# Kernel optimization log

Hardware: AMD Instinct MI355X
Metric: run time of the kernel (lower is better)

Reference implementation:

```python
import jax, jax.numpy as jnp
import numpy as np

FACTOR = 5


def setup_inputs() -> dict:
    key = jax.random.key(0)
    k1, k2, k3, k4 = jax.random.split(key, 4)
    B, L, H, D = 2, 4096, 8, 64
    sample_k = min(FACTOR * int(np.ceil(np.log(L))), L)  # 45
    return {
        "queries": jax.random.normal(k1, (B, L, H, D), dtype=jnp.float32),
        "keys": jax.random.normal(k2, (B, L, H, D), dtype=jnp.float32),
        "values": jax.random.normal(k3, (B, L, H, D), dtype=jnp.float32),
        "attn_mask": jnp.zeros((1,), dtype=bool),  # unused; ProbMask is built internally
        "index_sample": jax.random.randint(k4, (L, sample_k), 0, L, dtype=jnp.int32),
    }


def reference(queries, keys, values, attn_mask, index_sample):
    # queries/keys/values: [B, L, H, D] -> [B, H, L, D]
    Q = jnp.swapaxes(queries, 1, 2)
    K = jnp.swapaxes(keys, 1, 2)
    V = jnp.swapaxes(values, 1, 2)
    B, H, L_Q, D = Q.shape
    L_K = K.shape[2]
    n_top = min(FACTOR * int(np.ceil(np.log(L_Q))), L_Q)
    scale = 1.0 / jnp.sqrt(jnp.float32(D))

    # --- sparse measurement: sampled QK scores ---
    # K_sample[b,h,q,s,d] = K[b,h,index_sample[q,s],d]
    K_sample = K[:, :, index_sample, :]                       # [B,H,L_Q,S,D]
    QK_sample = jnp.einsum("bhqd,bhqsd->bhqs", Q, K_sample)   # [B,H,L_Q,S]
    M = QK_sample.max(axis=-1) - QK_sample.sum(axis=-1) / L_K  # sparsity measure

    # --- top-u query selection ---
    _, M_top = jax.lax.top_k(M, n_top)                         # [B,H,u]
    Q_reduce = jnp.take_along_axis(Q, M_top[..., None], axis=2)  # [B,H,u,D]

    # --- full scores for selected queries ---
    scores = jnp.einsum("bhud,bhkd->bhuk", Q_reduce, K) * scale  # [B,H,u,L_K]

    # mask_flag=True: causal ProbMask (key pos > selected query pos)
    key_pos = jnp.arange(L_K)
    causal = key_pos[None, None, None, :] > M_top[..., None]
    scores = jnp.where(causal, -jnp.inf, scores)
    attn = jax.nn.softmax(scores, axis=-1)

    # --- initial context (cumsum, masked case) + scatter update ---
    context = jnp.cumsum(V, axis=2)                            # [B,H,L_Q,D]
    ctx_sel = jnp.einsum("bhuk,bhkd->bhud", attn, V)
    b_idx = jnp.arange(B)[:, None, None]
    h_idx = jnp.arange(H)[None, :, None]
    context = context.at[b_idx, h_idx, M_top].set(ctx_sel)
    return jnp.swapaxes(context, 1, 2)  # [B, L_Q, H, D]
```

## Files before the change

kernel.cpp:

```cpp
#include <hip/hip_runtime.h>
#include <math.h>

#define B_    2
#define L_    4096
#define H_    8
#define D_    64
#define S_    45
#define NT_   45
#define BH_   16
#define CHV   64
#define NCHV  64
#define KC    128
#define NKC   32
#define SCALE 0.125f
#define NEG_BIG (-1e30f)

#define OFF_M     0
#define OFF_MTOP  65536
#define OFF_MPART 66304
#define OFF_SPART 89344
#define OFF_CTXP  112384
#define OFF_VSUM  1586944

template <int CTRL>
__device__ __forceinline__ float dpp_ror_f(float x) {
    int y = __builtin_amdgcn_update_dpp(0, __float_as_int(x), CTRL, 0xF, 0xF, false);
    return __int_as_float(y);
}

__device__ __forceinline__ unsigned short f2bf(float x) {
    return (unsigned short)(__float_as_uint(x) >> 16);
}
__device__ __forceinline__ float bflo(unsigned u) { return __uint_as_float(u << 16); }
__device__ __forceinline__ float bfhi(unsigned u) { return __uint_as_float(u & 0xffff0000u); }

__global__ __launch_bounds__(256) void k1(const float* __restrict__ Q,
                                          const float* __restrict__ Kt,
                                          const float* __restrict__ V,
                                          const int* __restrict__ samp,
                                          float* __restrict__ ws)
{
    int tid  = threadIdx.x;
    int w    = tid >> 6;
    int lane = tid & 63;

    if (blockIdx.x < 4096) {
        int i   = blockIdx.x;
        int xcd = i & 7;
        int b   = xcd >> 2;
        int hh  = (xcd >> 1) & 1;
        int qq  = ((i >> 3) << 1) | (xcd & 1);

        __shared__ int soff[4][S_];
        if (tid < 4 * S_) {
            int qs = tid / S_, ss = tid - qs * S_;
            soff[qs][ss] = (samp[(qq * 4 + qs) * S_ + ss] << 11) | (hh << 10);
        }
        __syncthreads();

        int q  = qq * 4 + w;
        int h4 = lane >> 4;

        const float4 q4 = *(const float4*)(Q +
            ((((long)b * L_ + q) * H_ + hh * 4) << 6) + lane * 4);

        const char* kslab = (const char*)Kt + (long)b * (L_ * 2048);
        unsigned lb = (unsigned)(lane * 16);

        float mx = NEG_BIG, sm = 0.f;
#pragma unroll
        for (int jb = 0; jb < 45; jb += 15) {
            float4 kb[15];
#pragma unroll
            for (int j = 0; j < 15; ++j)
                kb[j] = *(const float4*)(kslab +
                        ((unsigned)soff[w][jb + j] + lb));
#pragma unroll
            for (int j = 0; j < 15; ++j) {
                float p = q4.x * kb[j].x + q4.y * kb[j].y +
                          q4.z * kb[j].z + q4.w * kb[j].w;
                p += dpp_ror_f<0x121>(p);
                p += dpp_ror_f<0x122>(p);
                p += dpp_ror_f<0x124>(p);
                p += dpp_ror_f<0x128>(p);
                mx = fmaxf(mx, p);
                sm += p;
            }
        }
        if ((lane & 15) == 0)
            ws[OFF_M + ((long)(b * 8 + hh * 4 + h4)) * L_ + q] =
                mx - sm * (1.0f / (float)L_);
    } else {
        int unit = (blockIdx.x - 4096) * 4 + w;
        int bh = unit >> 6, ch = unit & 63;
        int b = bh >> 3, h = bh & 7;
        const float* vp = V + ((((long)b * L_ + (long)ch * CHV) * H_ + h) << 6) + lane;
        float ssum = 0.f;
#pragma unroll
        for (int ib = 0; ib < CHV; ib += 16) {
            float vb[16];
#pragma unroll
            for (int j = 0; j < 16; ++j) vb[j] = vp[(long)(ib + j) * (H_ * D_)];
#pragma unroll
            for (int j = 0; j < 16; ++j) ssum += vb[j];
        }
        ws[OFF_VSUM + unit * 64 + lane] = ssum;
    }
}

__global__ __launch_bounds__(256) void k2(float* __restrict__ ws)
{
    int tid  = threadIdx.x;
    int w    = tid >> 6;
    int lane = tid & 63;

    int bh = blockIdx.x;
    int* Mtop = (int*)ws + OFF_MTOP + bh * NT_;

    __shared__ float lv_[4][NT_];
    __shared__ int   li_[4][NT_];

    const float4* m4 = (const float4*)(ws + OFF_M + (long)bh * L_ +
                                       w * 1024 + lane * 16);
    float vals[16];
    {
        float4 a = m4[0], bq = m4[1], c = m4[2], d = m4[3];
        vals[0]=a.x; vals[1]=a.y; vals[2]=a.z; vals[3]=a.w;
        vals[4]=bq.x; vals[5]=bq.y; vals[6]=bq.z; vals[7]=bq.w;
        vals[8]=c.x; vals[9]=c.y; vals[10]=c.z; vals[11]=c.w;
        vals[12]=d.x; vals[13]=d.y; vals[14]=d.z; vals[15]=d.w;
    }
    float lv = NEG_BIG; int li = lane * 16;
#pragma unroll
    for (int j = 0; j < 16; ++j)
        if (vals[j] > lv) { lv = vals[j]; li = lane * 16 + j; }

    for (int r = 0; r < NT_; ++r) {
        float rm = lv;
        rm = fmaxf(rm, dpp_ror_f<0x121>(rm));
        rm = fmaxf(rm, dpp_ror_f<0x122>(rm));
        rm = fmaxf(rm, dpp_ror_f<0x124>(rm));
        rm = fmaxf(rm, dpp_ror_f<0x128>(rm));
        rm = fmaxf(rm, __shfl_xor(rm, 16));
        rm = fmaxf(rm, __shfl_xor(rm, 32));
        unsigned long long bm = __ballot(lv == rm);
        int winner = __ffsll(bm) - 1;
        int wi = __shfl(li, winner);
        if (lane == 0) { lv_[w][r] = rm; li_[w][r] = w * 1024 + wi; }
        if (lane == winner) {
#pragma unroll
            for (int j = 0; j < 16; ++j)
                if (j == (wi & 15)) vals[j] = NEG_BIG;
            lv = NEG_BIG; li = lane * 16;
#pragma unroll
            for (int j = 0; j < 16; ++j)
                if (vals[j] > lv) { lv = vals[j]; li = lane * 16 + j; }
        }
    }
    __syncthreads();

    if (w == 0) {
        int g = lane & 3;
        int p = 0;
        float hv = lv_[g][0]; int hi = li_[g][0];
        for (int r = 0; r < NT_; ++r) {
            float v0 = __shfl(hv, 0), v1 = __shfl(hv, 1),
                  v2 = __shfl(hv, 2), v3 = __shfl(hv, 3);
            int   i0 = __shfl(hi, 0), i1 = __shfl(hi, 1),
                  i2 = __shfl(hi, 2), i3 = __shfl(hi, 3);
            float bv = v0; int bi = i0, bg = 0;
            if (v1 > bv) { bv = v1; bi = i1; bg = 1; }
            if (v2 > bv) { bv = v2; bi = i2; bg = 2; }
            if (v3 > bv) { bv = v3; bi = i3; bg = 3; }
            if (lane == 0) Mtop[r] = bi;
            if (g == bg) {
                ++p;
                hv = (p < NT_) ? lv_[g][p] : NEG_BIG;
                hi = (p < NT_) ? li_[g][p] : 0;
            }
        }
    }
}

#define KPAD16 72
#define NUH    23
__global__ __launch_bounds__(256) void k3(const float* __restrict__ Q,
                                          const float* __restrict__ Kt,
                                          const float* __restrict__ V,
                                          float* __restrict__ out,
                                          float* __restrict__ ws)
{
    __shared__ unsigned short Klds16[KC * KPAD16];
    __shared__ unsigned short P16[NUH * KC];
    __shared__ int qpos[NUH];

    int tid = threadIdx.x;

    if (blockIdx.x < 1024) {
        int bh = blockIdx.x >> 6;
        int kc = (blockIdx.x >> 1) & 31;
        int ug = blockIdx.x & 1;
        int b = bh >> 3, h = bh & 7;
        int kbase = kc * KC;
        int u0 = ug * 23;
        int NU = ug ? 22 : 23;

        if (tid < NU) qpos[tid] = ((const int*)ws)[OFF_MTOP + bh * NT_ + tid + u0];

        {
            const float4* ksrc4 = (const float4*)(Kt + ((((long)b * L_ + kbase) * H_ + h) << 6));
#pragma unroll
            for (int i = 0; i < 8; ++i) {
                int e = i * 256 + tid;
                int r = e >> 4, c4 = e & 15;
                float4 kv = ksrc4[(long)r * (H_ * D_ / 4) + c4];
                uint2 pk;
                pk.x = (__float_as_uint(kv.x) >> 16) | (__float_as_uint(kv.y) & 0xffff0000u);
                pk.y = (__float_as_uint(kv.z) >> 16) | (__float_as_uint(kv.w) & 0xffff0000u);
                *(uint2*)&Klds16[r * KPAD16 + c4 * 4] = pk;
            }
        }
        __syncthreads();

        int k = tid & 127, uh = tid >> 7;
        int kpos = kbase + k;
        {
            float kf[64];
#pragma unroll
            for (int j = 0; j < 8; ++j) {
                uint4 U = *(const uint4*)&Klds16[k * KPAD16 + j * 8];
                kf[j*8+0] = bflo(U.x); kf[j*8+1] = bfhi(U.x);
                kf[j*8+2] = bflo(U.y); kf[j*8+3] = bfhi(U.y);
                kf[j*8+4] = bflo(U.z); kf[j*8+5] = bfhi(U.z);
                kf[j*8+6] = bflo(U.w); kf[j*8+7] = bfhi(U.w);
            }

#pragma unroll 3
            for (int j = 0; j < 12; ++j) {
                int ul = uh * 12 + j;
                if (ul > NU - 1) ul = NU - 1;
                int qp_ = __builtin_amdgcn_readfirstlane(qpos[ul]);
                const float4* qrow = (const float4*)(Q + ((((long)b * L_ + qp_) * H_ + h) << 6));
                float a0 = 0.f, a1 = 0.f, a2 = 0.f, a3 = 0.f;
#pragma unroll
                for (int jj = 0; jj < 16; jj += 4) {
                    float4 q0 = qrow[jj + 0], q1 = qrow[jj + 1];
                    float4 q2 = qrow[jj + 2], q3 = qrow[jj + 3];
                    a0 += q0.x * kf[jj*4+ 0] + q0.y * kf[jj*4+ 1] +
                          q0.z * kf[jj*4+ 2] + q0.w * kf[jj*4+ 3];
                    a1 += q1.x * kf[jj*4+ 4] + q1.y * kf[jj*4+ 5] +
                          q1.z * kf[jj*4+ 6] + q1.w * kf[jj*4+ 7];
                    a2 += q2.x * kf[jj*4+ 8] + q2.y * kf[jj*4+ 9] +
                          q2.z * kf[jj*4+10] + q2.w * kf[jj*4+11];
                    a3 += q3.x * kf[jj*4+12] + q3.y * kf[jj*4+13] +
                          q3.z * kf[jj*4+14] + q3.w * kf[jj*4+15];
                }
                float sc = ((a0 + a1) + (a2 + a3)) * SCALE;
                if (kpos > qp_) sc = NEG_BIG;
                P16[ul * KC + k] = f2bf(sc);
            }
        }
        __syncthreads();

        int lane = tid & 63, w = tid >> 6;
        for (int ul = w; ul < NU; ul += 4) {
            float s0 = bflo(P16[ul * KC + lane]);
            float s1 = bflo(P16[ul * KC + 64 + lane]);
            float m = fmaxf(s0, s1);
#pragma unroll
            for (int off = 32; off; off >>= 1) m = fmaxf(m, __shfl_xor(m, off));
            float e0 = __expf(s0 - m), e1 = __expf(s1 - m);
            unsigned short b0 = f2bf(e0), b1 = f2bf(e1);
            P16[ul * KC + lane]      = b0;
            P16[ul * KC + 64 + lane] = b1;
            float sm = bflo(b0) + bflo(b1);
#pragma unroll
            for (int off = 32; off; off >>= 1) sm += __shfl_xor(sm, off);
            if (lane == 0) {
                ws[OFF_MPART + ((long)bh * NT_ + u0 + ul) * NKC + kc] = m;
                ws[OFF_SPART + ((long)bh * NT_ + u0 + ul) * NKC + kc] = sm;
            }
        }
        __syncthreads();

        {
            const float* vsrc = V + ((((long)b * L_ + kbase) * H_ + h) << 6);
            float ctx[6];
#pragma unroll
            for (int j = 0; j < 6; ++j) ctx[j] = 0.f;
            for (int kk8 = 0; kk8 < 16; ++kk8) {
                float v[8];
#pragma unroll
                for (int t = 0; t < 8; ++t)
                    v[t] = vsrc[(long)(kk8 * 8 + t) * (H_ * D_) + lane];
#pragma unroll
                for (int j = 0; j < 6; ++j) {
                    int ul = w + j * 4;
                    if (ul < NU) {
                        uint4 U = *(const uint4*)&P16[ul * KC + kk8 * 8];
                        ctx[j] += bflo(U.x) * v[0] + bfhi(U.x) * v[1]
                                + bflo(U.y) * v[2] + bfhi(U.y) * v[3]
                                + bflo(U.z) * v[4] + bfhi(U.z) * v[5]
                                + bflo(U.w) * v[6] + bfhi(U.w) * v[7];
                    }
                }
            }
#pragma unroll
            for (int j = 0; j < 6; ++j) {
                int ul = w + j * 4;
                if (ul < NU)
                    ws[OFF_CTXP + ((long)(bh * NKC + kc) * NT_ + u0 + ul) * 64 + lane] = ctx[j];
            }
        }
    } else {
        int w    = tid >> 6;
        int lane = tid & 63;
        int unit = (blockIdx.x - 1024) * 4 + w;
        int bh = unit >> 6, ch = unit & 63;
        int b = bh >> 3, h = bh & 7;
        int d = lane;

        float acc = 0.f;
        {
            const float* vs = ws + OFF_VSUM + (long)bh * NCHV * 64 + d;
            int c = 0;
            for (; c + 8 <= ch; c += 8) {
                float vb[8];
#pragma unroll
                for (int j = 0; j < 8; ++j) vb[j] = vs[(c + j) * 64];
#pragma unroll
                for (int j = 0; j < 8; ++j) acc += vb[j];
            }
            for (; c < ch; ++c) acc += vs[c * 64];
        }

        const float* vp = V   + ((((long)b * L_ + (long)ch * CHV) * H_ + h) << 6) + d;
        float*       op = out + ((((long)b * L_ + (long)ch * CHV) * H_ + h) << 6) + d;
#pragma unroll
        for (int ib = 0; ib < CHV; ib += 16) {
            float vb[16];
#pragma unroll
            for (int j = 0; j < 16; ++j) vb[j] = vp[(long)(ib + j) * (H_ * D_)];
#pragma unroll
            for (int j = 0; j < 16; ++j) {
                acc += vb[j];
                op[(long)(ib + j) * (H_ * D_)] = acc;
            }
        }
    }
}

__global__ __launch_bounds__(64) void kD(float* __restrict__ out,
                                         const float* __restrict__ ws)
{
    int lane = threadIdx.x;
    int unit = blockIdx.x;
    int bh = unit / NT_, u = unit - bh * NT_;
    int b = bh >> 3, h = bh & 7;

    const float4* mp4 = (const float4*)(ws + OFF_MPART + ((long)bh * NT_ + u) * NKC);
    const float4* sp4 = (const float4*)(ws + OFF_SPART + ((long)bh * NT_ + u) * NKC);

    float mc[NKC], sc[NKC];
    float m = NEG_BIG;
#pragma unroll
    for (int c4 = 0; c4 < NKC / 4; ++c4) {
        float4 mv = mp4[c4];
        float4 sv = sp4[c4];
        mc[c4 * 4 + 0] = mv.x; mc[c4 * 4 + 1] = mv.y;
        mc[c4 * 4 + 2] = mv.z; mc[c4 * 4 + 3] = mv.w;
        sc[c4 * 4 + 0] = sv.x; sc[c4 * 4 + 1] = sv.y;
        sc[c4 * 4 + 2] = sv.z; sc[c4 * 4 + 3] = sv.w;
        m = fmaxf(m, fmaxf(fmaxf(mv.x, mv.y), fmaxf(mv.z, mv.w)));
    }
    float T = 0.f, ctx = 0.f;
#pragma unroll
    for (int c = 0; c < NKC; ++c) {
        float wgt = __expf(mc[c] - m);
        T   += sc[c] * wgt;
        ctx += ws[OFF_CTXP + ((long)(bh * NKC + c) * NT_ + u) * 64 + lane] * wgt;
    }
    int qp = ((const int*)ws)[OFF_MTOP + bh * NT_ + u];
    out[((((long)b * L_ + qp) * H_ + h) << 6) + lane] = ctx / T;
}

extern "C" void kernel_launch(void* const* d_in, const int* in_sizes, int n_in,
                              void* d_out, int out_size, void* d_ws, size_t ws_size,
                              hipStream_t stream)
{
    const float* Q    = (const float*)d_in[0];
    const float* K    = (const float*)d_in[1];
    const float* V    = (const float*)d_in[2];
    const int*   samp = (const int*)d_in[4];
    float* out = (float*)d_out;
    float* ws  = (float*)d_ws;

    k1<<<4352, 256, 0, stream>>>(Q, K, V, samp, ws);
    k2<<<16, 256, 0, stream>>>(ws);
    k3<<<1280, 256, 0, stream>>>(Q, K, V, out, ws);
    kD<<<720, 64, 0, stream>>>(out, ws);
}
```

Baseline: 188.0 us.

## Compute selected-query scores with bf16 MFMA and fuse softmax into registers

Replaces the scalar FMA Q·K score loop in k3 with bf16 MFMA 16x16x32 tiles, staging the selected Q rows in swizzled LDS alongside K. The softmax max and sum are computed directly on the MFMA accumulators, which removes one LDS pass and a barrier. Partial stats are now kept per 64-key half, so the partial buffers double in size and the combine kernel reads twice as many partials. This adds workspace traffic and bf16 rounding of Q in exchange for far less ALU work.

```diff
diff --git a/kernel.cpp b/kernel.cpp
--- a/kernel.cpp
+++ b/kernel.cpp
@@ -11,16 +11,19 @@
 #define CHV   64
 #define NCHV  64
 #define KC    128
-#define NKC   32
+#define NKC2  64
 #define SCALE 0.125f
 #define NEG_BIG (-1e30f)
 
 #define OFF_M     0
 #define OFF_MTOP  65536
 #define OFF_MPART 66304
-#define OFF_SPART 89344
-#define OFF_CTXP  112384
-#define OFF_VSUM  1586944
+#define OFF_SPART 112384
+#define OFF_CTXP  158464
+#define OFF_VSUM  3107584
+
+typedef __attribute__((ext_vector_type(8))) short s8b;
+typedef __attribute__((ext_vector_type(4))) float f32x4;
 
 template <int CTRL>
 __device__ __forceinline__ float dpp_ror_f(float x) {
@@ -28,8 +31,8 @@
     return __int_as_float(y);
 }
 
-__device__ __forceinline__ unsigned short f2bf(float x) {
-    return (unsigned short)(__float_as_uint(x) >> 16);
+__device__ __forceinline__ unsigned f2bf(float x) {
+    return (__float_as_uint(x) >> 16);
 }
 __device__ __forceinline__ float bflo(unsigned u) { return __uint_as_float(u << 16); }
 __device__ __forceinline__ float bfhi(unsigned u) { return __uint_as_float(u & 0xffff0000u); }
@@ -183,7 +186,7 @@
 }
 
 #define KPAD16 72
-#define NUH    23
+#define PSTR   136
 __global__ __launch_bounds__(256) void k3(const float* __restrict__ Q,
                                           const float* __restrict__ Kt,
                                           const float* __restrict__ V,
@@ -191,8 +194,9 @@
                                           float* __restrict__ ws)
 {
     __shared__ unsigned short Klds16[KC * KPAD16];
-    __shared__ unsigned short P16[NUH * KC];
-    __shared__ int qpos[NUH];
+    __shared__ unsigned short Qs16[32 * KPAD16];
+    __shared__ unsigned short P16[32 * PSTR];
+    __shared__ int qposs[32];
 
     int tid = threadIdx.x;
 
@@ -205,7 +209,11 @@
         int u0 = ug * 23;
         int NU = ug ? 22 : 23;
 
-        if (tid < NU) qpos[tid] = ((const int*)ws)[OFF_MTOP + bh * NT_ + tid + u0];
+        if (tid < 32) {
+            int uu = tid < NU ? tid : NU - 1;
+            qposs[tid] = ((const int*)ws)[OFF_MTOP + bh * NT_ + u0 + uu];
+        }
+        __syncthreads();
 
         {
             const float4* ksrc4 = (const float4*)(Kt + ((((long)b * L_ + kbase) * H_ + h) << 6));
@@ -217,78 +225,99 @@
                 uint2 pk;
                 pk.x = (__float_as_uint(kv.x) >> 16) | (__float_as_uint(kv.y) & 0xffff0000u);
                 pk.y = (__float_as_uint(kv.z) >> 16) | (__float_as_uint(kv.w) & 0xffff0000u);
-                *(uint2*)&Klds16[r * KPAD16 + c4 * 4] = pk;
+                *(uint2*)&Klds16[r * KPAD16 + ((c4 * 4) ^ ((r & 7) << 3))] = pk;
+            }
+#pragma unroll
+            for (int i = 0; i < 2; ++i) {
+                int e = i * 256 + tid;
+                int r = e >> 4, c4 = e & 15;
+                int qp = qposs[r];
+                const float4* qsrc4 = (const float4*)(Q + ((((long)b * L_ + qp) * H_ + h) << 6));
+                float4 qv = qsrc4[c4];
+                uint2 pk;
+                pk.x = (__float_as_uint(qv.x) >> 16) | (__float_as_uint(qv.y) & 0xffff0000u);
+                pk.y = (__float_as_uint(qv.z) >> 16) | (__float_as_uint(qv.w) & 0xffff0000u);
+                *(uint2*)&Qs16[r * KPAD16 + ((c4 * 4) ^ ((r & 7) << 3))] = pk;
             }
         }
         __syncthreads();
 
-        int k = tid & 127, uh = tid >> 7;
-        int kpos = kbase + k;
         {
-            float kf[64];
-#pragma unroll
-            for (int j = 0; j < 8; ++j) {
-                uint4 U = *(const uint4*)&Klds16[k * KPAD16 + j * 8];
-                kf[j*8+0] = bflo(U.x); kf[j*8+1] = bfhi(U.x);
-                kf[j*8+2] = bflo(U.y); kf[j*8+3] = bfhi(U.y);
-                kf[j*8+4] = bflo(U.z); kf[j*8+5] = bfhi(U.z);
-                kf[j*8+6] = bflo(U.w); kf[j*8+7] = bfhi(U.w);
-            }
-
-#pragma unroll 3
-            for (int j = 0; j < 12; ++j) {
-                int ul = uh * 12 + j;
-                if (ul > NU - 1) ul = NU - 1;
-                int qp_ = __builtin_amdgcn_readfirstlane(qpos[ul]);
-                const float4* qrow = (const float4*)(Q + ((((long)b * L_ + qp_) * H_ + h) << 6));
-                float a0 = 0.f, a1 = 0.f, a2 = 0.f, a3 = 0.f;
-#pragma unroll
-                for (int jj = 0; jj < 16; jj += 4) {
-                    float4 q0 = qrow[jj + 0], q1 = qrow[jj + 1];
-                    float4 q2 = qrow[jj + 2], q3 = qrow[jj + 3];
-                    a0 += q0.x * kf[jj*4+ 0] + q0.y * kf[jj*4+ 1] +
-                          q0.z * kf[jj*4+ 2] + q0.w * kf[jj*4+ 3];
-                    a1 += q1.x * kf[jj*4+ 4] + q1.y * kf[jj*4+ 5] +
-                          q1.z * kf[jj*4+ 6] + q1.w * kf[jj*4+ 7];
-                    a2 += q2.x * kf[jj*4+ 8] + q2.y * kf[jj*4+ 9] +
-                          q2.z * kf[jj*4+10] + q2.w * kf[jj*4+11];
-                    a3 += q3.x * kf[jj*4+12] + q3.y * kf[jj*4+13] +
-                          q3.z * kf[jj*4+14] + q3.w * kf[jj*4+15];
+            int lane = tid & 63, w = tid >> 6;
+            int c = lane & 15, hi = lane >> 4;
+            int t = w & 1, H = w >> 1;
+            int slot = t * 16 + c;
+            int qp = qposs[slot];
+
+            s8b bq0 = *(const s8b*)&Qs16[slot * KPAD16 + ((hi * 8) ^ ((slot & 7) << 3))];
+            s8b bq1 = *(const s8b*)&Qs16[slot * KPAD16 + ((32 + hi * 8) ^ ((slot & 7) << 3))];
+
+            f32x4 acc0 = {0.f,0.f,0.f,0.f}, acc1 = acc0, acc2 = acc0, acc3 = acc0;
+#define QK_TILE(MT, ACC)                                                      \
+            {                                                                 \
+                int kr = H * 64 + (MT) * 16 + c;                              \
+                s8b a0 = *(const s8b*)&Klds16[kr * KPAD16 +                   \
+                            ((hi * 8) ^ ((kr & 7) << 3))];                    \
+                s8b a1 = *(const s8b*)&Klds16[kr * KPAD16 +                   \
+                            ((32 + hi * 8) ^ ((kr & 7) << 3))];               \
+                ACC = __builtin_amdgcn_mfma_f32_16x16x32_bf16(a0, bq0, ACC, 0, 0, 0); \
+                ACC = __builtin_amdgcn_mfma_f32_16x16x32_bf16(a1, bq1, ACC, 0, 0, 0); \
+            }
+            QK_TILE(0, acc0)
+            QK_TILE(1, acc1)
+            QK_TILE(2, acc2)
+            QK_TILE(3, acc3)
+#undef QK_TILE
+
+            float sv[16];
+            float m = NEG_BIG;
+#pragma unroll
+            for (int mt = 0; mt < 4; ++mt) {
+                f32x4 a = mt == 0 ? acc0 : (mt == 1 ? acc1 : (mt == 2 ? acc2 : acc3));
+#pragma unroll
+                for (int reg = 0; reg < 4; ++reg) {
+                    float s = a[reg] * SCALE;
+                    int kpos = kbase + H * 64 + mt * 16 + hi * 4 + reg;
+                    if (kpos > qp) s = NEG_BIG;
+                    sv[mt * 4 + reg] = s;
+                    m = fmaxf(m, s);
                 }
-                float sc = ((a0 + a1) + (a2 + a3)) * SCALE;
-                if (kpos > qp_) sc = NEG_BIG;
-                P16[ul * KC + k] = f2bf(sc);
+            }
+            m = fmaxf(m, __shfl_xor(m, 16));
+            m = fmaxf(m, __shfl_xor(m, 32));
+            float ssum = 0.f;
+#pragma unroll
+            for (int j = 0; j < 16; ++j) {
+                float e = __expf(sv[j] - m);
+                sv[j] = e;
+                ssum += e;
+            }
+            ssum += __shfl_xor(ssum, 16);
+            ssum += __shfl_xor(ssum, 32);
+            if (hi == 0 && c < NU) {
+                int sl = t * 16 + c;
+                if (sl < NU) {
+                    ws[OFF_MPART + ((long)bh * NT_ + u0 + sl) * NKC2 + kc * 2 + H] = m;
+                    ws[OFF_SPART + ((long)bh * NT_ + u0 + sl) * NKC2 + kc * 2 + H] = ssum;
+                }
+            }
+#pragma unroll
+            for (int mt = 0; mt < 4; ++mt) {
+                uint2 pk;
+                pk.x = f2bf(sv[mt * 4 + 0]) | (f2bf(sv[mt * 4 + 1]) << 16);
+                pk.y = f2bf(sv[mt * 4 + 2]) | (f2bf(sv[mt * 4 + 3]) << 16);
+                *(uint2*)&P16[slot * PSTR + H * 64 + mt * 16 + hi * 4] = pk;
             }
         }
         __syncthreads();
 
-        int lane = tid & 63, w = tid >> 6;
-        for (int ul = w; ul < NU; ul += 4) {
-            float s0 = bflo(P16[ul * KC + lane]);
-            float s1 = bflo(P16[ul * KC + 64 + lane]);
-            float m = fmaxf(s0, s1);
-#pragma unroll
-            for (int off = 32; off; off >>= 1) m = fmaxf(m, __shfl_xor(m, off));
-            float e0 = __expf(s0 - m), e1 = __expf(s1 - m);
-            unsigned short b0 = f2bf(e0), b1 = f2bf(e1);
-            P16[ul * KC + lane]      = b0;
-            P16[ul * KC + 64 + lane] = b1;
-            float sm = bflo(b0) + bflo(b1);
-#pragma unroll
-            for (int off = 32; off; off >>= 1) sm += __shfl_xor(sm, off);
-            if (lane == 0) {
-                ws[OFF_MPART + ((long)bh * NT_ + u0 + ul) * NKC + kc] = m;
-                ws[OFF_SPART + ((long)bh * NT_ + u0 + ul) * NKC + kc] = sm;
-            }
-        }
-        __syncthreads();
-
         {
+            int lane = tid & 63, w = tid >> 6;
             const float* vsrc = V + ((((long)b * L_ + kbase) * H_ + h) << 6);
-            float ctx[6];
-#pragma unroll
-            for (int j = 0; j < 6; ++j) ctx[j] = 0.f;
-            for (int kk8 = 0; kk8 < 16; ++kk8) {
+            float c0[6], c1[6];
+#pragma unroll
+            for (int j = 0; j < 6; ++j) { c0[j] = 0.f; c1[j] = 0.f; }
+            for (int kk8 = 0; kk8 < 8; ++kk8) {
                 float v[8];
 #pragma unroll
                 for (int t = 0; t < 8; ++t)
@@ -297,19 +326,38 @@
                 for (int j = 0; j < 6; ++j) {
                     int ul = w + j * 4;
                     if (ul < NU) {
-                        uint4 U = *(const uint4*)&P16[ul * KC + kk8 * 8];
-                        ctx[j] += bflo(U.x) * v[0] + bfhi(U.x) * v[1]
-                                + bflo(U.y) * v[2] + bfhi(U.y) * v[3]
-                                + bflo(U.z) * v[4] + bfhi(U.z) * v[5]
-                                + bflo(U.w) * v[6] + bfhi(U.w) * v[7];
+                        uint4 U = *(const uint4*)&P16[ul * PSTR + kk8 * 8];
+                        c0[j] += bflo(U.x) * v[0] + bfhi(U.x) * v[1]
+                               + bflo(U.y) * v[2] + bfhi(U.y) * v[3]
+                               + bflo(U.z) * v[4] + bfhi(U.z) * v[5]
+                               + bflo(U.w) * v[6] + bfhi(U.w) * v[7];
                     }
                 }
             }
+            for (int kk8 = 8; kk8 < 16; ++kk8) {
+                float v[8];
+#pragma unroll
+                for (int t = 0; t < 8; ++t)
+                    v[t] = vsrc[(long)(kk8 * 8 + t) * (H_ * D_) + lane];
+#pragma unroll
+                for (int j = 0; j < 6; ++j) {
+                    int ul = w + j * 4;
+                    if (ul < NU) {
+                        uint4 U = *(const uint4*)&P16[ul * PSTR + kk8 * 8];
+                        c1[j] += bflo(U.x) * v[0] + bfhi(U.x) * v[1]
+                               + bflo(U.y) * v[2] + bfhi(U.y) * v[3]
+                               + bflo(U.z) * v[4] + bfhi(U.z) * v[5]
+                               + bflo(U.w) * v[6] + bfhi(U.w) * v[7];
+                    }
+                }
+            }
 #pragma unroll
             for (int j = 0; j < 6; ++j) {
                 int ul = w + j * 4;
-                if (ul < NU)
-                    ws[OFF_CTXP + ((long)(bh * NKC + kc) * NT_ + u0 + ul) * 64 + lane] = ctx[j];
+                if (ul < NU) {
+                    ws[OFF_CTXP + ((long)(bh * NKC2 + kc * 2 + 0) * NT_ + u0 + ul) * 64 + lane] = c0[j];
+                    ws[OFF_CTXP + ((long)(bh * NKC2 + kc * 2 + 1) * NT_ + u0 + ul) * 64 + lane] = c1[j];
+                }
             }
         }
     } else {
@@ -358,27 +406,30 @@
     int bh = unit / NT_, u = unit - bh * NT_;
     int b = bh >> 3, h = bh & 7;
 
-    const float4* mp4 = (const float4*)(ws + OFF_MPART + ((long)bh * NT_ + u) * NKC);
-    const float4* sp4 = (const float4*)(ws + OFF_SPART + ((long)bh * NT_ + u) * NKC);
-
-    float mc[NKC], sc[NKC];
+    const float4* mp4 = (const float4*)(ws + OFF_MPART + ((long)bh * NT_ + u) * NKC2);
+    const float4* sp4 = (const float4*)(ws + OFF_SPART + ((long)bh * NT_ + u) * NKC2);
+
+    float mall[NKC2];
     float m = NEG_BIG;
 #pragma unroll
-    for (int c4 = 0; c4 < NKC / 4; ++c4) {
+    for (int c4 = 0; c4 < NKC2 / 4; ++c4) {
         float4 mv = mp4[c4];
+        mall[c4 * 4 + 0] = mv.x; mall[c4 * 4 + 1] = mv.y;
+        mall[c4 * 4 + 2] = mv.z; mall[c4 * 4 + 3] = mv.w;
+        m = fmaxf(m, fmaxf(fmaxf(mv.x, mv.y), fmaxf(mv.z, mv.w)));
+    }
+    float T = 0.f, ctx = 0.f;
+#pragma unroll 4
+    for (int c4 = 0; c4 < NKC2 / 4; ++c4) {
         float4 sv = sp4[c4];
-        mc[c4 * 4 + 0] = mv.x; mc[c4 * 4 + 1] = mv.y;
-        mc[c4 * 4 + 2] = mv.z; mc[c4 * 4 + 3] = mv.w;
-        sc[c4 * 4 + 0] = sv.x; sc[c4 * 4 + 1] = sv.y;
-        sc[c4 * 4 + 2] = sv.z; sc[c4 * 4 + 3] = sv.w;
-        m = fmaxf(m, fmaxf(fmaxf(mv.x, mv.y), fmaxf(mv.z, mv.w)));
-    }
-    float T = 0.f, ctx = 0.f;
-#pragma unroll
-    for (int c = 0; c < NKC; ++c) {
-        float wgt = __expf(mc[c] - m);
-        T   += sc[c] * wgt;
-        ctx += ws[OFF_CTXP + ((long)(bh * NKC + c) * NT_ + u) * 64 + lane] * wgt;
+        float s4[4] = {sv.x, sv.y, sv.z, sv.w};
+#pragma unroll
+        for (int j = 0; j < 4; ++j) {
+            int c = c4 * 4 + j;
+            float wgt = __expf(mall[c] - m);
+            T   += s4[j] * wgt;
+            ctx += ws[OFF_CTXP + ((long)(bh * NKC2 + c) * NT_ + u) * 64 + lane] * wgt;
+        }
     }
     int qp = ((const int*)ws)[OFF_MTOP + bh * NT_ + u];
     out[((((long)b * L_ + qp) * H_ + h) << 6) + lane] = ctx / T;
```

Result: no change. 187.2 us (-0.5%).
